# Kernel optimization log

Measured on AMD Instinct MI355X. Metric: run time of the kernel, lower is better.

Reference implementation:

```python
import jax, jax.numpy as jnp
import numpy as np

C = 256      # in_channels
NH = 4       # n_heads
NG = 32      # GroupNorm num_groups
EPS = 1e-5   # torch GroupNorm default eps


def _conv1x1(x, w, b):
    # 1x1 conv == per-pixel channel matmul. x: (B,C,H,W), w: (O,C), b: (O,)
    return jnp.einsum('oc,bchw->bohw', w, x) + b[None, :, None, None]


def _groupnorm(x, gamma, beta):
    b, c, h, w = x.shape
    xg = x.reshape(b, NG, c // NG, h, w)
    mu = xg.mean(axis=(2, 3, 4), keepdims=True)
    var = xg.var(axis=(2, 3, 4), keepdims=True)
    xn = ((xg - mu) * jax.lax.rsqrt(var + EPS)).reshape(b, c, h, w)
    return xn * gamma[None, :, None, None] + beta[None, :, None, None]


def setup_inputs() -> dict:
    key = jax.random.key(0)
    ks = jax.random.split(key, 5)
    B, H, W = 2, 64, 64
    s = 1.0 / np.sqrt(C).astype(np.float32)
    return {
        'x': jax.random.normal(ks[0], (B, C, H, W), jnp.float32),
        'gamma': jnp.ones((C,), jnp.float32),
        'beta': jnp.zeros((C,), jnp.float32),
        'wq': jax.random.normal(ks[1], (C, C), jnp.float32) * s,
        'bq': jnp.zeros((C,), jnp.float32),
        'wk': jax.random.normal(ks[2], (C, C), jnp.float32) * s,
        'bk': jnp.zeros((C,), jnp.float32),
        'wv': jax.random.normal(ks[3], (C, C), jnp.float32) * s,
        'bv': jnp.zeros((C,), jnp.float32),
        'wp': jax.random.normal(ks[4], (C, C), jnp.float32) * s,
        'bp': jnp.zeros((C,), jnp.float32),
    }


def reference(x, gamma, beta, wq, bq, wk, bk, wv, bv, wp, bp):
    b, c, h, w = x.shape
    c_ = c // NH  # head dim
    hn = _groupnorm(x, gamma, beta)
    # NOTE: original splits channels as (head_dim, n_heads) with head_dim leading
    q = _conv1x1(hn, wq, bq).reshape(b, c_, NH, h * w)
    k = _conv1x1(hn, wk, bk).reshape(b, c_, NH, h * w)
    v = _conv1x1(hn, wv, bv).reshape(b, c_, NH, h * w)
    scores = jnp.einsum('bcnq,bcnk->bqkn', q, k) * (c_ ** -0.5)  # (B,S,S,NH)
    attn = jax.nn.softmax(scores, axis=2)  # softmax over key axis
    out = jnp.einsum('bcnd,bqdn->bcnq', v, attn).reshape(b, c, h, w)
    return x + _conv1x1(out, wp, bp)
```

## Files before the change

kernel.cpp:

```cpp
#include <hip/hip_runtime.h>

#define CH 256
#define NHEAD 4
#define HD 64
#define SP 4096
#define NB 2
#define QSCALE 0.1803368801111204f

typedef __attribute__((ext_vector_type(8))) short bf16x8;
typedef __attribute__((ext_vector_type(4))) float f32x4;
typedef unsigned int u32;
typedef unsigned short u16;

__device__ inline u16 b16(float f) {
    u32 u = __float_as_uint(f);
    return (u16)((u + 0x8000u) >> 16);
}
__device__ inline float fexp2(float x) { return __builtin_amdgcn_exp2f(x); }

__global__ __launch_bounds__(256) void prep_kernel(
    const float* __restrict__ x, float2* __restrict__ part,
    const float* __restrict__ wq, const float* __restrict__ wk,
    const float* __restrict__ wv, const float* __restrict__ wp,
    u16* __restrict__ wqb, u16* __restrict__ wkb,
    u16* __restrict__ wvb, u16* __restrict__ wpb)
{
    int tid = threadIdx.x;
    if (blockIdx.x < 256) {
        int bgq = blockIdx.x;
        int bg = bgq >> 2, qtr = bgq & 3;
        const float4* xp = (const float4*)(x + (size_t)bg * 8 * SP) + qtr * 2048;
        float s = 0.f, ss = 0.f;
        for (int i = tid; i < 2048; i += 256) {
            float4 u = xp[i];
            s  += (u.x + u.y) + (u.z + u.w);
            ss += (u.x * u.x + u.y * u.y) + (u.z * u.z + u.w * u.w);
        }
#pragma unroll
        for (int off = 32; off > 0; off >>= 1) {
            s  += __shfl_down(s, off);
            ss += __shfl_down(ss, off);
        }
        __shared__ float ws_s[4], ws_q[4];
        int w = tid >> 6;
        if ((tid & 63) == 0) { ws_s[w] = s; ws_q[w] = ss; }
        __syncthreads();
        if (tid == 0)
            part[bgq] = make_float2(ws_s[0] + ws_s[1] + ws_s[2] + ws_s[3],
                                    ws_q[0] + ws_q[1] + ws_q[2] + ws_q[3]);
    } else {
        int idx = (blockIdx.x - 256) * 256 + tid;
        int m = idx >> 16, i = idx & 65535;
        if (m == 0)      wqb[i] = b16(wq[i] * QSCALE);
        else if (m == 1) wkb[i] = b16(wk[i]);
        else if (m == 2) wvb[i] = b16(wv[i]);
        else {
            int c = i >> 8, col = i & 255;
            int n = col & 3, d = col >> 2;
            wpb[c * 256 + n * 64 + d] = b16(wp[i]);
        }
    }
}

__global__ __launch_bounds__(256) void qkv_gemm_kernel(
    const float* __restrict__ x, const float2* __restrict__ part,
    const float* __restrict__ gamma, const float* __restrict__ beta,
    const u16* __restrict__ wqb, const u16* __restrict__ wkb,
    const u16* __restrict__ wvb,
    const float* __restrict__ bq, const float* __restrict__ bk,
    const float* __restrict__ bv,
    u16* __restrict__ qt, u16* __restrict__ ktp, u16* __restrict__ vtp)
{
    int zz = blockIdx.y;
    int b = zz / 3, p = zz % 3;
    const u16* W = (p == 0) ? wqb : (p == 1) ? wkb : wvb;
    const float* bias = (p == 0) ? bq : (p == 1) ? bk : bv;
    float bs = (p == 0) ? QSCALE : 1.f;
    int s0 = blockIdx.x * 32;
    int tid = threadIdx.x, w = tid >> 6, lane = tid & 63;
    int t = lane >> 4, ln = lane & 15;

    __shared__ u16 SB[10240];
    __shared__ float As[256], Bs[256];

    {
        int c = tid, bg = b * 32 + (c >> 3);
        float s = 0.f, ss = 0.f;
#pragma unroll
        for (int q = 0; q < 4; q++) { float2 pp = part[bg * 4 + q]; s += pp.x; ss += pp.y; }
        float mu = s * (1.f / 32768.f);
        float var = ss * (1.f / 32768.f) - mu * mu;
        float rs = rsqrtf(var + 1e-5f);
        float ga = gamma[c];
        As[c] = rs * ga;
        Bs[c] = beta[c] - mu * rs * ga;
    }
    __syncthreads();

    {
        int cb = tid >> 3, sseg = (tid & 7) * 4;
#pragma unroll
        for (int it = 0; it < 8; it++) {
            int c = it * 32 + cb;
            float4 v = *(const float4*)&x[((size_t)b * CH + c) * SP + s0 + sseg];
            float aa = As[c], bb = Bs[c];
            SB[(sseg + 0) * 264 + c] = b16(fmaf(aa, v.x, bb));
            SB[(sseg + 1) * 264 + c] = b16(fmaf(aa, v.y, bb));
            SB[(sseg + 2) * 264 + c] = b16(fmaf(aa, v.z, bb));
            SB[(sseg + 3) * 264 + c] = b16(fmaf(aa, v.w, bb));
        }
    }
    __syncthreads();

    f32x4 acc[4][2];
#pragma unroll
    for (int og = 0; og < 4; og++)
#pragma unroll
        for (int sg = 0; sg < 2; sg++)
            acc[og][sg] = (f32x4){0.f, 0.f, 0.f, 0.f};

#pragma unroll
    for (int ks = 0; ks < 8; ks++) {
        bf16x8 af[4], bfv[2];
#pragma unroll
        for (int og = 0; og < 4; og++)
            af[og] = *(const bf16x8*)&W[(size_t)(w * 64 + og * 16 + ln) * CH + ks * 32 + t * 8];
#pragma unroll
        for (int sg = 0; sg < 2; sg++)
            bfv[sg] = *(const bf16x8*)&SB[(sg * 16 + ln) * 264 + ks * 32 + t * 8];
#pragma unroll
        for (int og = 0; og < 4; og++)
#pragma unroll
            for (int sg = 0; sg < 2; sg++)
                acc[og][sg] = __builtin_amdgcn_mfma_f32_16x16x32_bf16(
                    af[og], bfv[sg], acc[og][sg], 0, 0, 0);
    }
    __syncthreads();

    if (p < 2) {
#pragma unroll
        for (int og = 0; og < 4; og++)
#pragma unroll
            for (int sg = 0; sg < 2; sg++)
#pragma unroll
                for (int r = 0; r < 4; r++) {
                    int o = w * 64 + og * 16 + 4 * t + r;
                    SB[(r * 32 + sg * 16 + ln) * 72 + (w * 16 + og * 4 + t)] =
                        b16(acc[og][sg][r] + bias[o] * bs);
                }
        __syncthreads();
        if (p == 0) {
#pragma unroll
            for (int it = 0; it < 4; it++) {
                int f = it * 256 + tid;
                int o8 = f & 7, sl = (f >> 3) & 31, n = f >> 8;
                *(uint4*)&qt[((size_t)(b * 4 + n) * SP + s0 + sl) * HD + o8 * 8] =
                    *(const uint4*)&SB[(n * 32 + sl) * 72 + o8 * 8];
            }
        } else {
#pragma unroll
            for (int it = 0; it < 4; it++) {
                int f = it * 256 + tid;
                int o8 = f & 7, sl = (f >> 3) & 31, n = f >> 8;
                int key = s0 + sl;
                int g = ((key >> 4) & 3) * 2 + (o8 >> 2);
                int lp = (key & 15) + 16 * (o8 & 3);
                *(uint4*)&ktp[(size_t)(b * 4 + n) * SP * HD +
                              (size_t)(key >> 6) * 4096 + g * 512 + lp * 8] =
                    *(const uint4*)&SB[(n * 32 + sl) * 72 + o8 * 8];
            }
        }
    } else {
#pragma unroll
        for (int og = 0; og < 4; og++)
#pragma unroll
            for (int sg = 0; sg < 2; sg++)
#pragma unroll
                for (int r = 0; r < 4; r++) {
                    int o = w * 64 + og * 16 + 4 * t + r;
                    SB[(r * 64 + w * 16 + og * 4 + t) * 40 + sg * 16 + ln] =
                        b16(acc[og][sg][r] + bias[o]);
                }
        __syncthreads();
#pragma unroll
        for (int it = 0; it < 4; it++) {
            int f = it * 256 + tid;
            int so8 = f & 3, d = (f >> 2) & 63, n = f >> 8;
            int key = s0 + so8 * 8;
            int g = ((d >> 4) & 3) * 2 + ((key >> 5) & 1);
            int lp = (d & 15) + 16 * ((key >> 3) & 3);
            *(uint4*)&vtp[(size_t)(b * 4 + n) * SP * HD +
                          (size_t)(key >> 6) * 4096 + g * 512 + lp * 8] =
                *(const uint4*)&SB[(n * 64 + d) * 40 + so8 * 8];
        }
    }
}

template <int NT>
__global__ __launch_bounds__(512) void attn_kernel(
    const u16* __restrict__ qtb, const u16* __restrict__ ktp,
    const u16* __restrict__ vtp, u16* __restrict__ opart,
    float* __restrict__ lpart)
{
    int bx = blockIdx.x;
    int z = bx & 7, qt_i = (bx >> 3) & 15, sp = bx >> 7;
    int sq0 = qt_i * 256;
    int tile0 = sp * NT;
    const u16* qz = qtb + (size_t)z * SP * HD;
    const u16* kz = ktp + (size_t)z * SP * HD;
    const u16* vz = vtp + (size_t)z * SP * HD;

    int tid = threadIdx.x, w = tid >> 6, l = tid & 63;
    int t = l >> 4, ln = l & 15;

    __shared__ __align__(16) u32 Pb[8][2][512];

    bf16x8 qf[2][2];
#pragma unroll
    for (int qg = 0; qg < 2; qg++)
#pragma unroll
        for (int ds = 0; ds < 2; ds++)
            qf[qg][ds] = *(const bf16x8*)&qz[
                (size_t)(sq0 + w * 32 + qg * 16 + ln) * HD + ds * 32 + t * 8];

    bf16x8 kf[8], vf[8];
#pragma unroll
    for (int g = 0; g < 8; g++)
        kf[g] = *(const bf16x8*)&kz[(size_t)tile0 * 4096 + g * 512 + l * 8];

    float lsum[2] = {0.f, 0.f};
    f32x4 oacc[2][4];
#pragma unroll
    for (int qg = 0; qg < 2; qg++)
#pragma unroll
        for (int dg = 0; dg < 4; dg++)
            oacc[qg][dg] = (f32x4){0.f, 0.f, 0.f, 0.f};

    const f32x4 z4 = {0.f, 0.f, 0.f, 0.f};
    f32x4 sa[2][4];

    auto ep = [&](int qg) {
#pragma unroll
        for (int kg = 0; kg < 4; kg++) {
            float e0 = fexp2(sa[qg][kg][0]);
            float e1 = fexp2(sa[qg][kg][1]);
            float e2 = fexp2(sa[qg][kg][2]);
            float e3 = fexp2(sa[qg][kg][3]);
            lsum[qg] += (e0 + e1) + (e2 + e3);
            u32 p0 = __builtin_amdgcn_perm(__float_as_uint(e1), __float_as_uint(e0), 0x07060302u);
            u32 p1 = __builtin_amdgcn_perm(__float_as_uint(e3), __float_as_uint(e2), 0x07060302u);
            int Lt = ln + 16 * (2 * (kg & 1) + (t >> 1));
            int ksg = kg >> 1;
            *(uint2*)&Pb[w][qg][(ksg * 64 + Lt) * 4 + 2 * (t & 1)] =
                make_uint2(p0, p1);
        }
    };

#pragma unroll
    for (int kti = 0; kti < NT; kti++) {
        size_t tb = (size_t)(tile0 + kti) * 4096;

        __syncthreads();

#pragma unroll
        for (int g = 0; g < 8; g++)
            vf[g] = *(const bf16x8*)&vz[tb + g * 512 + l * 8];

#pragma unroll
        for (int kg = 0; kg < 4; kg++)
#pragma unroll
            for (int qg = 0; qg < 2; qg++)
                sa[qg][kg] = __builtin_amdgcn_mfma_f32_16x16x32_bf16(
                    kf[kg * 2 + 0], qf[qg][0], z4, 0, 0, 0);
#pragma unroll
        for (int kg = 0; kg < 4; kg++)
#pragma unroll
            for (int qg = 0; qg < 2; qg++)
                sa[qg][kg] = __builtin_amdgcn_mfma_f32_16x16x32_bf16(
                    kf[kg * 2 + 1], qf[qg][1], sa[qg][kg], 0, 0, 0);

        if (kti < NT - 1) {
            size_t nb = tb + 4096;
#pragma unroll
            for (int g = 0; g < 8; g++)
                kf[g] = *(const bf16x8*)&kz[nb + g * 512 + l * 8];
        }

        ep(0);
#pragma unroll
        for (int qg = 0; qg < 2; qg++) {
            if (qg == 0) ep(1);
            bf16x8 pf[2];
#pragma unroll
            for (int ksg = 0; ksg < 2; ksg++)
                pf[ksg] = *(const bf16x8*)&Pb[w][qg][(ksg * 64 + l) * 4];
#pragma unroll
            for (int ksg = 0; ksg < 2; ksg++)
#pragma unroll
                for (int dg = 0; dg < 4; dg++)
                    oacc[qg][dg] = __builtin_amdgcn_mfma_f32_16x16x32_bf16(
                        pf[ksg], vf[dg * 2 + ksg], oacc[qg][dg], 0, 0, 0);
        }
    }

#pragma unroll
    for (int qg = 0; qg < 2; qg++) {
        lsum[qg] += __shfl_xor(lsum[qg], 16);
        lsum[qg] += __shfl_xor(lsum[qg], 32);
    }

    size_t obase = (size_t)(sp * 8 + z) * SP;
    u16* po = (u16*)&Pb[w][0][0];
#pragma unroll
    for (int qg = 0; qg < 2; qg++)
#pragma unroll
        for (int dg = 0; dg < 4; dg++)
#pragma unroll
            for (int r = 0; r < 4; r++)
                po[(qg * 16 + 4 * t + r) * 64 + dg * 16 + ln] = b16(oacc[qg][dg][r]);
#pragma unroll
    for (int i = 0; i < 4; i++) {
        int f = i * 512 + l * 8;
        int qloc = f >> 6, d0 = f & 63;
        uint4 v = *(const uint4*)&po[f];
        *(uint4*)&opart[(obase + sq0 + w * 32 + qloc) * HD + d0] = v;
    }
    if (t == 0)
#pragma unroll
        for (int qg = 0; qg < 2; qg++)
            lpart[obase + sq0 + w * 32 + qg * 16 + ln] = lsum[qg];
}

template <int NSPLIT>
__global__ __launch_bounds__(256) void proj_gemm_kernel(
    const u16* __restrict__ opart, const float* __restrict__ lpart,
    const u16* __restrict__ wpb, const float* __restrict__ bp,
    const float* __restrict__ x, float* __restrict__ out)
{
    int b = blockIdx.y;
    int s0 = blockIdx.x * 16;
    int tid = threadIdx.x, w = tid >> 6, lane = tid & 63;
    int t = lane >> 4, ln = lane & 15;

    __shared__ u16 BsL[16 * 264];

#pragma unroll
    for (int it = 0; it < 2; it++) {
        int f = it * 256 + tid;
        int oct = f & 31, s = f >> 5;
        int n = oct >> 3, d0 = (oct & 7) * 8;
        float lsumv = 0.f;
        float accv[8] = {0.f,0.f,0.f,0.f,0.f,0.f,0.f,0.f};
#pragma unroll
        for (int sp = 0; sp < NSPLIT; sp++) {
            size_t base = (size_t)(sp * 8 + b * 4 + n) * SP + s0 + s;
            lsumv += lpart[base];
            uint4 o4 = *(const uint4*)&opart[base * HD + d0];
            u32 ov[4] = {o4.x, o4.y, o4.z, o4.w};
#pragma unroll
            for (int i = 0; i < 4; i++) {
                accv[2 * i + 0] += __uint_as_float(ov[i] << 16);
                accv[2 * i + 1] += __uint_as_float(ov[i] & 0xffff0000u);
            }
        }
        float inv = 1.f / lsumv;
        u32 res[4];
#pragma unroll
        for (int i = 0; i < 4; i++) {
            u16 rl = b16(accv[2 * i + 0] * inv);
            u16 rh = b16(accv[2 * i + 1] * inv);
            res[i] = ((u32)rh << 16) | rl;
        }
        *(uint4*)&BsL[s * 264 + oct * 8] = make_uint4(res[0], res[1], res[2], res[3]);
    }
    __syncthreads();

    f32x4 acc[4];
#pragma unroll
    for (int og = 0; og < 4; og++)
        acc[og] = (f32x4){0.f, 0.f, 0.f, 0.f};

#pragma unroll
    for (int ks = 0; ks < 8; ks++) {
        bf16x8 af[4];
#pragma unroll
        for (int og = 0; og < 4; og++)
            af[og] = *(const bf16x8*)&wpb[(size_t)(w * 64 + og * 16 + ln) * CH + ks * 32 + t * 8];
        bf16x8 bfv = *(const bf16x8*)&BsL[ln * 264 + ks * 32 + t * 8];
#pragma unroll
        for (int og = 0; og < 4; og++)
            acc[og] = __builtin_amdgcn_mfma_f32_16x16x32_bf16(
                af[og], bfv, acc[og], 0, 0, 0);
    }

#pragma unroll
    for (int og = 0; og < 4; og++)
#pragma unroll
        for (int r = 0; r < 4; r++) {
            int c = w * 64 + og * 16 + 4 * t + r;
            size_t idx = ((size_t)b * CH + c) * SP + s0 + ln;
            out[idx] = acc[og][r] + bp[c] + x[idx];
        }
}

extern "C" void kernel_launch(void* const* d_in, const int* in_sizes, int n_in,
                              void* d_out, int out_size, void* d_ws, size_t ws_size,
                              hipStream_t stream)
{
    const float* x     = (const float*)d_in[0];
    const float* gamma = (const float*)d_in[1];
    const float* beta  = (const float*)d_in[2];
    const float* wq = (const float*)d_in[3]; const float* bq = (const float*)d_in[4];
    const float* wk = (const float*)d_in[5]; const float* bk = (const float*)d_in[6];
    const float* wv = (const float*)d_in[7]; const float* bv = (const float*)d_in[8];
    const float* wp = (const float*)d_in[9]; const float* bp = (const float*)d_in[10];
    float* out = (float*)d_out;

    const size_t TEN = (size_t)8 * SP * HD;
    char* wsb = (char*)d_ws;
    float2* part = (float2*)wsb;
    u16* wqb = (u16*)(wsb + 4096);
    u16* wkb = wqb + 65536;
    u16* wvb = wkb + 65536;
    u16* wpb = wvb + 65536;
    u16* qt  = wpb + 65536;
    u16* ktp = qt + TEN;
    u16* vtp = ktp + TEN;
    u16* opart = vtp + TEN;
    float* lpart = (float*)(opart + (size_t)4 * TEN);

    prep_kernel<<<dim3(1280), dim3(256), 0, stream>>>(
        x, part, wq, wk, wv, wp, wqb, wkb, wvb, wpb);
    qkv_gemm_kernel<<<dim3(128, 6), dim3(256), 0, stream>>>(
        x, part, gamma, beta, wqb, wkb, wvb, bq, bk, bv, qt, ktp, vtp);
    attn_kernel<16><<<dim3(512), dim3(512), 0, stream>>>(
        qt, ktp, vtp, opart, lpart);
    proj_gemm_kernel<4><<<dim3(256, 2), dim3(256), 0, stream>>>(
        opart, lpart, wpb, bp, x, out);
}
```

Baseline: 163.7 us.

## Shrink attention blocks, raise key split count, pack bf16 pairs in stores

Attention blocks drop from 512 to 256 threads, each covering 128 queries, and when the workspace is large enough the key dimension is split 8 ways instead of 4. That gives a 2048-block grid with launch bounds asking for 3 blocks per CU, and the per-tile __syncthreads is removed. The aim is more parallelism and occupancy for the attention stage, paid for with more partial outputs that the projection kernel must reduce. The QKV-GEMM normalisation store and the projection combine now write two bf16 values per 32-bit store via a packing helper, cutting LDS store count.

New measurement: 155.0 us. 1.06x faster.

```diff
diff --git a/kernel.cpp b/kernel.cpp
--- a/kernel.cpp
+++ b/kernel.cpp
@@ -15,6 +15,10 @@
 __device__ inline u16 b16(float f) {
     u32 u = __float_as_uint(f);
     return (u16)((u + 0x8000u) >> 16);
+}
+__device__ inline u32 bpack(float lo, float hi) {
+    u32 ul = __float_as_uint(lo), uh = __float_as_uint(hi);
+    return ((uh + 0x8000u) & 0xffff0000u) | ((ul + 0x8000u) >> 16);
 }
 __device__ inline float fexp2(float x) { return __builtin_amdgcn_exp2f(x); }
 
@@ -98,16 +102,21 @@
     __syncthreads();
 
     {
-        int cb = tid >> 3, sseg = (tid & 7) * 4;
-#pragma unroll
-        for (int it = 0; it < 8; it++) {
-            int c = it * 32 + cb;
-            float4 v = *(const float4*)&x[((size_t)b * CH + c) * SP + s0 + sseg];
-            float aa = As[c], bb = Bs[c];
-            SB[(sseg + 0) * 264 + c] = b16(fmaf(aa, v.x, bb));
-            SB[(sseg + 1) * 264 + c] = b16(fmaf(aa, v.y, bb));
-            SB[(sseg + 2) * 264 + c] = b16(fmaf(aa, v.z, bb));
-            SB[(sseg + 3) * 264 + c] = b16(fmaf(aa, v.w, bb));
+        int c2 = (tid >> 3) * 2;
+        int sseg = (tid & 7) * 4;
+#pragma unroll
+        for (int it = 0; it < 4; it++) {
+            int c = it * 64 + c2;
+            float4 v0 = *(const float4*)&x[((size_t)b * CH + c) * SP + s0 + sseg];
+            float4 v1 = *(const float4*)&x[((size_t)b * CH + c + 1) * SP + s0 + sseg];
+            float a0 = As[c], b0 = Bs[c], a1 = As[c + 1], b1 = Bs[c + 1];
+            float e0[4] = {fmaf(a0, v0.x, b0), fmaf(a0, v0.y, b0),
+                           fmaf(a0, v0.z, b0), fmaf(a0, v0.w, b0)};
+            float e1[4] = {fmaf(a1, v1.x, b1), fmaf(a1, v1.y, b1),
+                           fmaf(a1, v1.z, b1), fmaf(a1, v1.w, b1)};
+#pragma unroll
+            for (int j = 0; j < 4; j++)
+                *(u32*)&SB[(sseg + j) * 264 + c] = bpack(e0[j], e1[j]);
         }
     }
     __syncthreads();
@@ -197,14 +206,14 @@
 }
 
 template <int NT>
-__global__ __launch_bounds__(512) void attn_kernel(
+__global__ __launch_bounds__(256, 3) void attn_kernel(
     const u16* __restrict__ qtb, const u16* __restrict__ ktp,
     const u16* __restrict__ vtp, u16* __restrict__ opart,
     float* __restrict__ lpart)
 {
     int bx = blockIdx.x;
-    int z = bx & 7, qt_i = (bx >> 3) & 15, sp = bx >> 7;
-    int sq0 = qt_i * 256;
+    int z = bx & 7, qt_i = (bx >> 3) & 31, sp = bx >> 8;
+    int sq0 = qt_i * 128;
     int tile0 = sp * NT;
     const u16* qz = qtb + (size_t)z * SP * HD;
     const u16* kz = ktp + (size_t)z * SP * HD;
@@ -213,7 +222,7 @@
     int tid = threadIdx.x, w = tid >> 6, l = tid & 63;
     int t = l >> 4, ln = l & 15;
 
-    __shared__ __align__(16) u32 Pb[8][2][512];
+    __shared__ __align__(16) u32 Pb[4][2][512];
 
     bf16x8 qf[2][2];
 #pragma unroll
@@ -260,8 +269,6 @@
     for (int kti = 0; kti < NT; kti++) {
         size_t tb = (size_t)(tile0 + kti) * 4096;
 
-        __syncthreads();
-
 #pragma unroll
         for (int g = 0; g < 8; g++)
             vf[g] = *(const bf16x8*)&vz[tb + g * 512 + l * 8];
@@ -366,11 +373,8 @@
         float inv = 1.f / lsumv;
         u32 res[4];
 #pragma unroll
-        for (int i = 0; i < 4; i++) {
-            u16 rl = b16(accv[2 * i + 0] * inv);
-            u16 rh = b16(accv[2 * i + 1] * inv);
-            res[i] = ((u32)rh << 16) | rl;
-        }
+        for (int i = 0; i < 4; i++)
+            res[i] = (bpack(accv[2 * i + 0] * inv, accv[2 * i + 1] * inv));
         *(uint4*)&BsL[s * 264 + oct * 8] = make_uint4(res[0], res[1], res[2], res[3]);
     }
     __syncthreads();
@@ -417,6 +421,9 @@
     float* out = (float*)d_out;
 
     const size_t TEN = (size_t)8 * SP * HD;
+    const size_t NEED8 = 4096 + 524288 + 3 * TEN * 2 + 8 * TEN * 2 + 8 * 8 * SP * 4;
+    int nsplit = (ws_size >= NEED8) ? 8 : 4;
+
     char* wsb = (char*)d_ws;
     float2* part = (float2*)wsb;
     u16* wqb = (u16*)(wsb + 4096);
@@ -427,14 +434,21 @@
     u16* ktp = qt + TEN;
     u16* vtp = ktp + TEN;
     u16* opart = vtp + TEN;
-    float* lpart = (float*)(opart + (size_t)4 * TEN);
+    float* lpart = (float*)(opart + (size_t)nsplit * TEN);
 
     prep_kernel<<<dim3(1280), dim3(256), 0, stream>>>(
         x, part, wq, wk, wv, wp, wqb, wkb, wvb, wpb);
     qkv_gemm_kernel<<<dim3(128, 6), dim3(256), 0, stream>>>(
         x, part, gamma, beta, wqb, wkb, wvb, bq, bk, bv, qt, ktp, vtp);
-    attn_kernel<16><<<dim3(512), dim3(512), 0, stream>>>(
-        qt, ktp, vtp, opart, lpart);
-    proj_gemm_kernel<4><<<dim3(256, 2), dim3(256), 0, stream>>>(
-        opart, lpart, wpb, bp, x, out);
-}
+    if (nsplit == 8) {
+        attn_kernel<8><<<dim3(2048), dim3(256), 0, stream>>>(
+            qt, ktp, vtp, opart, lpart);
+        proj_gemm_kernel<8><<<dim3(256, 2), dim3(256), 0, stream>>>(
+            opart, lpart, wpb, bp, x, out);
+    } else {
+        attn_kernel<16><<<dim3(1024), dim3(256), 0, stream>>>(
+            qt, ktp, vtp, opart, lpart);
+        proj_gemm_kernel<4><<<dim3(256, 2), dim3(256), 0, stream>>>(
+            opart, lpart, wpb, bp, x, out);
+    }
+}
```
